# Kernel optimization log

Hardware: AMD Instinct MI355X
Metric: run time of the kernel (lower is better)

Reference implementation:

```python
import jax, jax.numpy as jnp
import numpy as np

N = 50000      # nodes
E = 800000     # edges
G = 64         # graphs in batch
DIN = 128
H = 128
DOUT = 128
EPS = 1e-5     # BatchNorm eps
SLOPE = 0.01   # leaky_relu negative slope


def setup_inputs() -> dict:
    key = jax.random.key(0)
    ks = jax.random.split(key, 12)
    x = jax.random.normal(ks[0], (N, DIN), jnp.float32)
    edge_index = jax.random.randint(ks[1], (2, E), 0, N)
    batch = jnp.sort(jax.random.randint(ks[2], (N,), 0, G))
    edge_weight = jax.random.uniform(ks[3], (E,), jnp.float32)

    def lin(k, i, o):
        return (jax.random.normal(k, (i, o), jnp.float32) / np.float32(np.sqrt(i)))

    W0, b0 = lin(ks[4], DIN, H), jnp.zeros((H,), jnp.float32)
    W1, b1 = lin(ks[5], H, H), jnp.zeros((H,), jnp.float32)
    W2, b2 = lin(ks[6], H, DOUT), jnp.zeros((DOUT,), jnp.float32)
    # BatchNorm (eval mode): affine params + running stats
    g0, be0 = jnp.ones((H,), jnp.float32), jnp.zeros((H,), jnp.float32)
    m0 = 0.1 * jax.random.normal(ks[7], (H,), jnp.float32)
    v0 = jax.random.uniform(ks[8], (H,), jnp.float32, minval=0.5, maxval=1.5)
    g1, be1 = jnp.ones((H,), jnp.float32), jnp.zeros((H,), jnp.float32)
    m1 = 0.1 * jax.random.normal(ks[9], (H,), jnp.float32)
    v1 = jax.random.uniform(ks[10], (H,), jnp.float32, minval=0.5, maxval=1.5)
    return dict(x=x, edge_weight=edge_weight, W0=W0, b0=b0, W1=W1, b1=b1,
                W2=W2, b2=b2, g0=g0, be0=be0, m0=m0, v0=v0,
                g1=g1, be1=be1, m1=m1, v1=v1,
                edge_index=edge_index, batch=batch)


def _gcn_conv(x, src, dst, w, W, b):
    # PyG GCNConv: x' = D^{-1/2}(A + I)D^{-1/2} (x W) + b, self-loop weight 1.
    x = x @ W                                   # [N, out]
    deg = jax.ops.segment_sum(w, dst, num_segments=N)          # [N]
    safe = jnp.where(deg > 0, deg, 1.0)
    dinv = jnp.where(deg > 0, 1.0 / jnp.sqrt(safe), 0.0)        # deg^{-1/2}, inf->0
    norm = dinv[src] * w * dinv[dst]                             # [E+N]
    msgs = x[src] * norm[:, None]                                # [E+N, out]
    return jax.ops.segment_sum(msgs, dst, num_segments=N) + b


def _bn_eval(x, g, b, m, v):
    return (x - m) * jax.lax.rsqrt(v + EPS) * g + b


def _leaky(x):
    return jnp.where(x > 0, x, SLOPE * x)


def reference(x, edge_weight, W0, b0, W1, b1, W2, b2,
              g0, be0, m0, v0, g1, be1, m1, v1, edge_index, batch):
    loops = jnp.arange(N)
    src = jnp.concatenate([edge_index[0], loops])
    dst = jnp.concatenate([edge_index[1], loops])
    w = jnp.concatenate([edge_weight, jnp.ones((N,), edge_weight.dtype)])

    h = _leaky(_bn_eval(_gcn_conv(x, src, dst, w, W0, b0), g0, be0, m0, v0))
    h = _leaky(_bn_eval(_gcn_conv(h, src, dst, w, W1, b1), g1, be1, m1, v1))
    h = _gcn_conv(h, src, dst, w, W2, b2)                        # [N, DOUT]

    # global_mean_pool over batch assignment
    sums = jax.ops.segment_sum(h, batch, num_segments=G)         # [G, DOUT]
    cnt = jax.ops.segment_sum(jnp.ones((N,), h.dtype), batch, num_segments=G)
    return sums / jnp.clip(cnt, 1.0)[:, None]
```

## Files before the change

kernel.cpp:

```cpp
#include <hip/hip_runtime.h>

#define EPS 1e-5f
#define SLOPE 0.01f
#define FIXP 262144.0f
#define RSTRIDE 64

typedef short short8 __attribute__((ext_vector_type(8)));
typedef float f32x4 __attribute__((ext_vector_type(4)));
typedef float f32x2 __attribute__((ext_vector_type(2)));

static __device__ __forceinline__ unsigned short f32_to_bf16(float x){
  unsigned int u = __float_as_uint(x);
  unsigned int r = u + 0x7FFFu + ((u >> 16) & 1u);
  return (unsigned short)(r >> 16);
}
static __device__ __forceinline__ float bf16lo_to_f32(unsigned int v){
  return __uint_as_float(v << 16);
}
static __device__ __forceinline__ float bf16hi_to_f32(unsigned int v){
  return __uint_as_float(v & 0xFFFF0000u);
}


__global__ void k_packzero(const float* __restrict__ W0, const float* __restrict__ W1,
                           const float* __restrict__ W2, short* __restrict__ Bh,
                           short* __restrict__ Bl, unsigned int* __restrict__ cnt,
                           int n){
  if ((int)blockIdx.x >= 192){
    int idx = ((int)blockIdx.x - 192)*256 + threadIdx.x;
    if (idx < n) cnt[idx] = 0u;
    return;
  }
  int idx = blockIdx.x*256 + threadIdx.x;
  int which = idx >> 14;
  int r = idx & 16383;
  const float* W = (which == 0) ? W0 : ((which == 1) ? W1 : W2);
  int j = r & 7;
  int l = (r >> 3) & 63;
  int s = (r >> 9) & 3;
  int t = r >> 11;
  int k = s*32 + ((l >> 4) << 3) + j;
  int nn = t*16 + (l & 15);
  float v = W[k*128 + nn];
  unsigned short hb = f32_to_bf16(v);
  float hf = bf16lo_to_f32(hb);
  unsigned short lb = f32_to_bf16(v - hf);
  Bh[idx] = (short)hb;
  Bl[idx] = (short)lb;
}


__global__ __launch_bounds__(256) void k_fused0(
    const int* __restrict__ dst, const float* __restrict__ ew,
    unsigned int* __restrict__ cnt, int* __restrict__ pwr, int E, int cntB,
    const float* __restrict__ X, const short* __restrict__ Bh,
    const short* __restrict__ Bl, unsigned short* __restrict__ Y, int nrows){
  int bid = (int)blockIdx.x;
  if (bid < cntB){
    int e = bid*256 + (int)threadIdx.x;
    if (e < E){
      unsigned int add = (1u << 24) | (unsigned int)(ew[e] * FIXP);
      unsigned int old = atomicAdd(&cnt[dst[e]], add);
      pwr[e] = (int)(old >> 24);
    }
    return;
  }
  int w    = threadIdx.x >> 6;
  int lane = threadIdx.x & 63;
  int m    = lane & 15;
  int kg   = lane >> 4;
  int row0 = (bid - cntB)*64 + w*16;

  f32x4 acc[8];
  #pragma unroll
  for (int t = 0; t < 8; ++t) acc[t] = (f32x4){0.f, 0.f, 0.f, 0.f};

  int arow = row0 + m;
  if (arow >= nrows) arow = nrows - 1;
  const float* ap0 = X + (size_t)arow*128 + (kg << 3);
  const short8* bh0 = (const short8*)Bh + lane;
  const short8* bl0 = (const short8*)Bl + lane;

  #pragma unroll
  for (int s = 0; s < 4; ++s){
    const float* ap = ap0 + s*32;
    float4 a0 = *(const float4*)ap;
    float4 a1 = *(const float4*)(ap + 4);
    float av[8] = {a0.x, a0.y, a0.z, a0.w, a1.x, a1.y, a1.z, a1.w};
    short8 ah, al;
    #pragma unroll
    for (int j = 0; j < 8; ++j){
      unsigned short hb = f32_to_bf16(av[j]);
      float hf = bf16lo_to_f32(hb);
      ah[j] = (short)hb;
      al[j] = (short)f32_to_bf16(av[j] - hf);
    }
    #pragma unroll
    for (int t = 0; t < 8; ++t){
      short8 bh = bh0[t*256 + s*64];
      short8 bl = bl0[t*256 + s*64];
      acc[t] = __builtin_amdgcn_mfma_f32_16x16x32_bf16(ah, bh, acc[t], 0, 0, 0);
      acc[t] = __builtin_amdgcn_mfma_f32_16x16x32_bf16(al, bh, acc[t], 0, 0, 0);
      acc[t] = __builtin_amdgcn_mfma_f32_16x16x32_bf16(ah, bl, acc[t], 0, 0, 0);
    }
  }
  #pragma unroll
  for (int t = 0; t < 8; ++t){
    #pragma unroll
    for (int r = 0; r < 4; ++r){
      int grow = row0 + (kg << 2) + r;
      if (grow < nrows) Y[(size_t)grow*128 + t*16 + m] = f32_to_bf16(acc[t][r]);
    }
  }
}


__global__ void k_fill(const int* __restrict__ src, const int* __restrict__ dst,
                       const float* __restrict__ w, const int* __restrict__ pwr,
                       const unsigned int* __restrict__ cnt,
                       int2* __restrict__ csr, int E){
  int e = blockIdx.x*blockDim.x + threadIdx.x;
  if (e >= E) return;
  int d = dst[e], s = src[e];
  int slot = pwr[e];
  unsigned int cd = cnt[d], cs = cnt[s];
  float dgd = 1.0f + (float)(cd & 0xFFFFFFu) * (1.0f/FIXP);
  float dgs = 1.0f + (float)(cs & 0xFFFFFFu) * (1.0f/FIXP);
  float nr = rsqrtf(dgd) * rsqrtf(dgs) * w[e];
  if (slot < RSTRIDE)
    csr[((size_t)d << 6) + slot] = make_int2(s, __float_as_int(nr));
}


#define ACC4(v, nn) \
  acc[0] += (f32x2){bf16lo_to_f32((v).x), bf16hi_to_f32((v).x)} * (nn); \
  acc[1] += (f32x2){bf16lo_to_f32((v).y), bf16hi_to_f32((v).y)} * (nn); \
  acc[2] += (f32x2){bf16lo_to_f32((v).z), bf16hi_to_f32((v).z)} * (nn); \
  acc[3] += (f32x2){bf16lo_to_f32((v).w), bf16hi_to_f32((v).w)} * (nn);

template<bool BN>
__global__ __launch_bounds__(256) void k_gather(
    const unsigned short* __restrict__ Y, const unsigned int* __restrict__ cnt,
    const int2* __restrict__ csr,
    const float* __restrict__ bias,
    const float* __restrict__ gam, const float* __restrict__ bet,
    const float* __restrict__ mean, const float* __restrict__ var,
    unsigned int* __restrict__ outv, int n){
  int wid  = (blockIdx.x * blockDim.x + threadIdx.x) >> 6;
  int lane = threadIdx.x & 63;
  if (wid >= n) return;
  int g = lane >> 4;
  int q = lane & 15;

  unsigned int cw = cnt[wid];
  int len = (int)(cw >> 24);
  if (len > RSTRIDE) len = RSTRIDE;
  int lenr = (len + 15) & ~15;

  int cex = 0, cey = 0;
  if (lane < lenr){
    int2 ce = csr[((size_t)wid << 6) + lane];
    cex = ce.x; cey = ce.y;
  }

  f32x2 acc[4];
  #pragma unroll
  for (int j = 0; j < 4; ++j) acc[j] = (f32x2){0.f, 0.f};

  const char* Yb = (const char*)Y;

  for (int base = 0; base < len; base += 16){
    #pragma unroll
    for (int u = 0; u < 4; ++u){
      int j = base + g*4 + u;
      bool valid = j < len;
      int sj = __shfl(cex, j, 64);
      int nj = __shfl(cey, j, 64);
      unsigned su = valid ? (unsigned)sj : 0u;
      float nr = valid ? __int_as_float(nj) : 0.f;
      uint4 v = *(const uint4*)(Yb + ((size_t)su << 8) + (q << 4));
      ACC4(v, nr);
    }
  }

  float s[8] = {acc[0].x, acc[0].y, acc[1].x, acc[1].y,
                acc[2].x, acc[2].y, acc[3].x, acc[3].y};
  #pragma unroll
  for (int j = 0; j < 8; ++j){
    s[j] += __shfl_xor(s[j], 16, 64);
    s[j] += __shfl_xor(s[j], 32, 64);
  }

  if (g == 0){
    uint4 v = *(const uint4*)(Yb + ((size_t)wid << 8) + (q << 4));
    float dg = 1.0f + (float)(cw & 0xFFFFFFu) * (1.0f/FIXP);
    float sf = 1.0f / dg;
    s[0] += bf16lo_to_f32(v.x)*sf; s[1] += bf16hi_to_f32(v.x)*sf;
    s[2] += bf16lo_to_f32(v.y)*sf; s[3] += bf16hi_to_f32(v.y)*sf;
    s[4] += bf16lo_to_f32(v.z)*sf; s[5] += bf16hi_to_f32(v.z)*sf;
    s[6] += bf16lo_to_f32(v.w)*sf; s[7] += bf16hi_to_f32(v.w)*sf;

    int c = q << 3;
    float4 bi0 = *(const float4*)&bias[c];
    float4 bi1 = *(const float4*)&bias[c+4];
    float o[8] = {s[0]+bi0.x, s[1]+bi0.y, s[2]+bi0.z, s[3]+bi0.w,
                  s[4]+bi1.x, s[5]+bi1.y, s[6]+bi1.z, s[7]+bi1.w};
    if (BN){
      float4 ga0 = *(const float4*)&gam[c],  ga1 = *(const float4*)&gam[c+4];
      float4 bt0 = *(const float4*)&bet[c],  bt1 = *(const float4*)&bet[c+4];
      float4 mn0 = *(const float4*)&mean[c], mn1 = *(const float4*)&mean[c+4];
      float4 vr0 = *(const float4*)&var[c],  vr1 = *(const float4*)&var[c+4];
      float gv[8] = {ga0.x,ga0.y,ga0.z,ga0.w, ga1.x,ga1.y,ga1.z,ga1.w};
      float bv[8] = {bt0.x,bt0.y,bt0.z,bt0.w, bt1.x,bt1.y,bt1.z,bt1.w};
      float mv[8] = {mn0.x,mn0.y,mn0.z,mn0.w, mn1.x,mn1.y,mn1.z,mn1.w};
      float vv[8] = {vr0.x,vr0.y,vr0.z,vr0.w, vr1.x,vr1.y,vr1.z,vr1.w};
      #pragma unroll
      for (int j = 0; j < 8; ++j){
        float a = gv[j] * rsqrtf(vv[j] + EPS);
        float tt = (o[j] - mv[j]) * a + bv[j];
        o[j] = tt > 0.f ? tt : SLOPE*tt;
      }
    }
    unsigned int p0 = ((unsigned int)f32_to_bf16(o[1]) << 16) | f32_to_bf16(o[0]);
    unsigned int p1 = ((unsigned int)f32_to_bf16(o[3]) << 16) | f32_to_bf16(o[2]);
    unsigned int p2 = ((unsigned int)f32_to_bf16(o[5]) << 16) | f32_to_bf16(o[4]);
    unsigned int p3 = ((unsigned int)f32_to_bf16(o[7]) << 16) | f32_to_bf16(o[6]);
    *(uint4*)((char*)outv + ((size_t)wid << 8) + (q << 4)) = make_uint4(p0,p1,p2,p3);
  }
}


__global__ __launch_bounds__(256) void k_gemm_bf16(const unsigned short* __restrict__ Xb,
                                                   const short* __restrict__ Bh,
                                                   const short* __restrict__ Bl,
                                                   unsigned short* __restrict__ Y,
                                                   int nrows){
  int w    = threadIdx.x >> 6;
  int lane = threadIdx.x & 63;
  int m    = lane & 15;
  int kg   = lane >> 4;
  int row0 = blockIdx.x*64 + w*16;

  f32x4 acc[8];
  #pragma unroll
  for (int t = 0; t < 8; ++t) acc[t] = (f32x4){0.f, 0.f, 0.f, 0.f};

  int arow = row0 + m;
  if (arow >= nrows) arow = nrows - 1;
  const short8* ap = (const short8*)(Xb + (size_t)arow*128) + kg;
  const short8* bh0 = (const short8*)Bh + lane;
  const short8* bl0 = (const short8*)Bl + lane;

  #pragma unroll
  for (int s = 0; s < 4; ++s){
    short8 a = ap[s*4];
    #pragma unroll
    for (int t = 0; t < 8; ++t){
      acc[t] = __builtin_amdgcn_mfma_f32_16x16x32_bf16(a, bh0[t*256 + s*64], acc[t], 0, 0, 0);
      acc[t] = __builtin_amdgcn_mfma_f32_16x16x32_bf16(a, bl0[t*256 + s*64], acc[t], 0, 0, 0);
    }
  }
  #pragma unroll
  for (int t = 0; t < 8; ++t){
    #pragma unroll
    for (int r = 0; r < 4; ++r){
      int grow = row0 + (kg << 2) + r;
      if (grow < nrows) Y[(size_t)grow*128 + t*16 + m] = f32_to_bf16(acc[t][r]);
    }
  }
}


__global__ void k_pool(const unsigned int* __restrict__ h, const int* __restrict__ batch,
                       float* __restrict__ out, int n){
  __shared__ float2 red[1024];
  __shared__ int ss[2];
  int g = blockIdx.x;
  if (threadIdx.x < 2){
    int target = g + (int)threadIdx.x;
    int lo = 0, hi = n;
    while (lo < hi){ int mid = (lo + hi) >> 1; if (batch[mid] < target) lo = mid + 1; else hi = mid; }
    ss[threadIdx.x] = lo;
  }
  __syncthreads();
  int a = ss[0], b = ss[1];
  int rg = threadIdx.x >> 6;
  int c2 = threadIdx.x & 63;
  float sx = 0.f, sy = 0.f;
  for (int i = a + rg; i < b; i += 16){
    unsigned int v = h[((size_t)i << 6) + c2];
    sx += bf16lo_to_f32(v);
    sy += bf16hi_to_f32(v);
  }
  red[threadIdx.x] = make_float2(sx, sy);
  __syncthreads();
  if (rg == 0){
    float tx = 0.f, ty = 0.f;
    #pragma unroll
    for (int k = 0; k < 16; ++k){
      float2 r = red[c2 + k*64];
      tx += r.x; ty += r.y;
    }
    int cn = b - a;
    float inv = 1.0f / (float)(cn > 0 ? cn : 1);
    out[g*128 + 2*c2]     = tx * inv;
    out[g*128 + 2*c2 + 1] = ty * inv;
  }
}


extern "C" void kernel_launch(void* const* d_in, const int* in_sizes, int n_in,
                              void* d_out, int out_size, void* d_ws, size_t ws_size,
                              hipStream_t stream) {
  const int N = in_sizes[0] / 128;
  const int E = in_sizes[1];
  const int G = out_size / 128;
  const int NB = (N + 255) / 256;
  const int CB = (E + 255) / 256;
  const int GB = (N + 63) / 64;

  const float* x   = (const float*)d_in[0];
  const float* ew  = (const float*)d_in[1];
  const float* W0  = (const float*)d_in[2];
  const float* b0  = (const float*)d_in[3];
  const float* W1  = (const float*)d_in[4];
  const float* b1  = (const float*)d_in[5];
  const float* W2  = (const float*)d_in[6];
  const float* b2  = (const float*)d_in[7];
  const float* g0  = (const float*)d_in[8];
  const float* be0 = (const float*)d_in[9];
  const float* m0  = (const float*)d_in[10];
  const float* v0  = (const float*)d_in[11];
  const float* g1  = (const float*)d_in[12];
  const float* be1 = (const float*)d_in[13];
  const float* m1  = (const float*)d_in[14];
  const float* v1  = (const float*)d_in[15];
  const int*   ei  = (const int*)d_in[16];
  const int*   bat = (const int*)d_in[17];
  float* out = (float*)d_out;

  char* p = (char*)d_ws;
  auto alloc = [&](size_t bytes)->char*{
    char* q = p; p += (bytes + 255) & ~(size_t)255; return q;
  };
  unsigned int* cnt = (unsigned int*)alloc((size_t)N*4);
  int*   pwr    = (int*)  alloc((size_t)E*4);
  int2*  csr    = (int2*) alloc((size_t)N*RSTRIDE*8);
  unsigned short* Y  = (unsigned short*)alloc((size_t)N*128*2);
  unsigned short* Hb = (unsigned short*)alloc((size_t)N*128*2);
  short* Bh = (short*)alloc(3*16384*2);
  short* Bl = (short*)alloc(3*16384*2);

  const int* src = ei;
  const int* dst = ei + E;

  k_packzero<<<192 + NB, 256, 0, stream>>>(W0, W1, W2, Bh, Bl, cnt, N);
  k_fused0<<<CB + GB, 256, 0, stream>>>(dst, ew, cnt, pwr, E, CB, x, Bh, Bl, Y, N);
  k_fill  <<<CB, 256, 0, stream>>>(src, dst, ew, pwr, cnt, csr, E);

  k_gather<true><<<(N+3)/4, 256, 0, stream>>>(Y, cnt, csr,
                                              b0, g0, be0, m0, v0, (unsigned int*)Hb, N);
  k_gemm_bf16<<<GB, 256, 0, stream>>>(Hb, Bh + 16384, Bl + 16384, Y, N);
  k_gather<true><<<(N+3)/4, 256, 0, stream>>>(Y, cnt, csr,
                                              b1, g1, be1, m1, v1, (unsigned int*)Hb, N);
  k_gemm_bf16<<<GB, 256, 0, stream>>>(Hb, Bh + 32768, Bl + 32768, Y, N);
  k_gather<false><<<(N+3)/4, 256, 0, stream>>>(Y, cnt, csr,
                                               b2, nullptr, nullptr, nullptr, nullptr,
                                               (unsigned int*)Hb, N);
  k_pool<<<G, 1024, 0, stream>>>((const unsigned int*)Hb, bat, out, N);
}
```

Measured before the change: 240.7 us.

## Rebalance kernel fusion: separate atomics, fuse CSR fill with GEMM, two nodes per gather wave

The degree/slot atomic pass becomes its own kernel with four edges per thread, and the CSR fill is merged into the first GEMM launch. Both use nontemporal loads and stores. The gather kernel now handles two destination nodes per wavefront and issues both nodes' row loads before accumulating, which raises memory-level parallelism. The costs are higher register pressure in the gather and load imbalance when neighbour counts differ between the paired nodes.

```diff
diff --git a/kernel.cpp b/kernel.cpp
--- a/kernel.cpp
+++ b/kernel.cpp
@@ -50,26 +50,57 @@
 }
 
 
-__global__ __launch_bounds__(256) void k_fused0(
+__global__ __launch_bounds__(256) void k_atomic(
     const int* __restrict__ dst, const float* __restrict__ ew,
-    unsigned int* __restrict__ cnt, int* __restrict__ pwr, int E, int cntB,
+    unsigned int* __restrict__ cnt, int* __restrict__ pwr, int E){
+  int base = blockIdx.x*1024 + (int)threadIdx.x;
+  #pragma unroll
+  for (int u = 0; u < 4; ++u){
+    int e = base + u*256;
+    if (e < E){
+      unsigned int add = (1u << 24) | (unsigned int)(ew[e] * FIXP);
+      unsigned int old = atomicAdd(&cnt[dst[e]], add);
+      __builtin_nontemporal_store((int)(old >> 24), pwr + e);
+    }
+  }
+}
+
+
+__global__ __launch_bounds__(256) void k_fillgemm(
+    const int* __restrict__ src, const int* __restrict__ dst,
+    const float* __restrict__ w, const int* __restrict__ pwr,
+    const unsigned int* __restrict__ cnt, long long* __restrict__ csr,
+    int E, int fillB,
     const float* __restrict__ X, const short* __restrict__ Bh,
     const short* __restrict__ Bl, unsigned short* __restrict__ Y, int nrows){
   int bid = (int)blockIdx.x;
-  if (bid < cntB){
-    int e = bid*256 + (int)threadIdx.x;
-    if (e < E){
-      unsigned int add = (1u << 24) | (unsigned int)(ew[e] * FIXP);
-      unsigned int old = atomicAdd(&cnt[dst[e]], add);
-      pwr[e] = (int)(old >> 24);
+  if (bid < fillB){
+    #pragma unroll
+    for (int u = 0; u < 2; ++u){
+      int e = bid*512 + u*256 + (int)threadIdx.x;
+      if (e < E){
+        int d = __builtin_nontemporal_load(dst + e);
+        int s = __builtin_nontemporal_load(src + e);
+        int slot = __builtin_nontemporal_load(pwr + e);
+        float wv = __builtin_nontemporal_load(w + e);
+        unsigned int cd = cnt[d], cs = cnt[s];
+        float dgd = 1.0f + (float)(cd & 0xFFFFFFu) * (1.0f/FIXP);
+        float dgs = 1.0f + (float)(cs & 0xFFFFFFu) * (1.0f/FIXP);
+        float nr = rsqrtf(dgd) * rsqrtf(dgs) * wv;
+        if (slot < RSTRIDE){
+          long long pk = ((long long)(unsigned)__float_as_int(nr) << 32) |
+                         (unsigned long long)(unsigned)s;
+          __builtin_nontemporal_store(pk, csr + ((size_t)d << 6) + slot);
+        }
+      }
     }
     return;
   }
-  int w    = threadIdx.x >> 6;
+  int wv2  = threadIdx.x >> 6;
   int lane = threadIdx.x & 63;
   int m    = lane & 15;
   int kg   = lane >> 4;
-  int row0 = (bid - cntB)*64 + w*16;
+  int row0 = (bid - fillB)*64 + wv2*16;
 
   f32x4 acc[8];
   #pragma unroll
@@ -115,24 +146,7 @@
 }
 
 
-__global__ void k_fill(const int* __restrict__ src, const int* __restrict__ dst,
-                       const float* __restrict__ w, const int* __restrict__ pwr,
-                       const unsigned int* __restrict__ cnt,
-                       int2* __restrict__ csr, int E){
-  int e = blockIdx.x*blockDim.x + threadIdx.x;
-  if (e >= E) return;
-  int d = dst[e], s = src[e];
-  int slot = pwr[e];
-  unsigned int cd = cnt[d], cs = cnt[s];
-  float dgd = 1.0f + (float)(cd & 0xFFFFFFu) * (1.0f/FIXP);
-  float dgs = 1.0f + (float)(cs & 0xFFFFFFu) * (1.0f/FIXP);
-  float nr = rsqrtf(dgd) * rsqrtf(dgs) * w[e];
-  if (slot < RSTRIDE)
-    csr[((size_t)d << 6) + slot] = make_int2(s, __float_as_int(nr));
-}
-
-
-#define ACC4(v, nn) \
+#define ACC4V(acc, v, nn) \
   acc[0] += (f32x2){bf16lo_to_f32((v).x), bf16hi_to_f32((v).x)} * (nn); \
   acc[1] += (f32x2){bf16lo_to_f32((v).y), bf16hi_to_f32((v).y)} * (nn); \
   acc[2] += (f32x2){bf16lo_to_f32((v).z), bf16hi_to_f32((v).z)} * (nn); \
@@ -146,52 +160,81 @@
     const float* __restrict__ gam, const float* __restrict__ bet,
     const float* __restrict__ mean, const float* __restrict__ var,
     unsigned int* __restrict__ outv, int n){
-  int wid  = (blockIdx.x * blockDim.x + threadIdx.x) >> 6;
+  int wv   = (blockIdx.x*256 + threadIdx.x) >> 6;
   int lane = threadIdx.x & 63;
-  if (wid >= n) return;
+  int nA = wv << 1;
+  if (nA >= n) return;
+  int nB = nA + 1;
+  bool hasB = nB < n;
   int g = lane >> 4;
   int q = lane & 15;
 
-  unsigned int cw = cnt[wid];
-  int len = (int)(cw >> 24);
-  if (len > RSTRIDE) len = RSTRIDE;
-  int lenr = (len + 15) & ~15;
-
-  int cex = 0, cey = 0;
-  if (lane < lenr){
-    int2 ce = csr[((size_t)wid << 6) + lane];
-    cex = ce.x; cey = ce.y;
-  }
-
-  f32x2 acc[4];
-  #pragma unroll
-  for (int j = 0; j < 4; ++j) acc[j] = (f32x2){0.f, 0.f};
+  unsigned int cwA = cnt[nA];
+  unsigned int cwB = hasB ? cnt[nB] : 0u;
+  int lenA = (int)(cwA >> 24); if (lenA > RSTRIDE) lenA = RSTRIDE;
+  int lenB = (int)(cwB >> 24); if (lenB > RSTRIDE) lenB = RSTRIDE;
+
+  int axs = 0, ays = 0, bxs = 0, bys = 0;
+  if (lane < lenA){ int2 e = csr[((size_t)nA << 6) + lane]; axs = e.x; ays = e.y; }
+  if (lane < lenB){ int2 e = csr[((size_t)nB << 6) + lane]; bxs = e.x; bys = e.y; }
+
+  f32x2 aA[4], aB[4];
+  #pragma unroll
+  for (int j = 0; j < 4; ++j){ aA[j] = (f32x2){0.f,0.f}; aB[j] = (f32x2){0.f,0.f}; }
 
   const char* Yb = (const char*)Y;
-
-  for (int base = 0; base < len; base += 16){
+  int lenM = lenA > lenB ? lenA : lenB;
+
+  for (int base = 0; base < lenM; base += 16){
+    uint4 vA[4], vB[4];
+    float nrA[4], nrB[4];
     #pragma unroll
     for (int u = 0; u < 4; ++u){
       int j = base + g*4 + u;
-      bool valid = j < len;
-      int sj = __shfl(cex, j, 64);
-      int nj = __shfl(cey, j, 64);
-      unsigned su = valid ? (unsigned)sj : 0u;
-      float nr = valid ? __int_as_float(nj) : 0.f;
-      uint4 v = *(const uint4*)(Yb + ((size_t)su << 8) + (q << 4));
-      ACC4(v, nr);
-    }
-  }
-
-  float s[8] = {acc[0].x, acc[0].y, acc[1].x, acc[1].y,
-                acc[2].x, acc[2].y, acc[3].x, acc[3].y};
+      {
+        bool val = j < lenA;
+        int sj = __shfl(axs, j, 64);
+        int nj = __shfl(ays, j, 64);
+        unsigned su = val ? (unsigned)sj : 0u;
+        nrA[u] = val ? __int_as_float(nj) : 0.f;
+        vA[u] = *(const uint4*)(Yb + ((size_t)su << 8) + (q << 4));
+      }
+      {
+        bool val = j < lenB;
+        int sj = __shfl(bxs, j, 64);
+        int nj = __shfl(bys, j, 64);
+        unsigned su = val ? (unsigned)sj : 0u;
+        nrB[u] = val ? __int_as_float(nj) : 0.f;
+        vB[u] = *(const uint4*)(Yb + ((size_t)su << 8) + (q << 4));
+      }
+    }
+    #pragma unroll
+    for (int u = 0; u < 4; ++u){
+      ACC4V(aA, vA[u], nrA[u]);
+      ACC4V(aB, vB[u], nrB[u]);
+    }
+  }
+
+  float sA[8] = {aA[0].x, aA[0].y, aA[1].x, aA[1].y,
+                 aA[2].x, aA[2].y, aA[3].x, aA[3].y};
+  float sB[8] = {aB[0].x, aB[0].y, aB[1].x, aB[1].y,
+                 aB[2].x, aB[2].y, aB[3].x, aB[3].y};
   #pragma unroll
   for (int j = 0; j < 8; ++j){
-    s[j] += __shfl_xor(s[j], 16, 64);
-    s[j] += __shfl_xor(s[j], 32, 64);
-  }
-
-  if (g == 0){
+    sA[j] += __shfl_xor(sA[j], 16, 64);
+    sA[j] += __shfl_xor(sA[j], 32, 64);
+    sB[j] += __shfl_xor(sB[j], 16, 64);
+    sB[j] += __shfl_xor(sB[j], 32, 64);
+  }
+
+  if (g == 0 || (g == 1 && hasB)){
+    bool isB = (g == 1);
+    int wid = isB ? nB : nA;
+    unsigned int cw = isB ? cwB : cwA;
+    float s[8];
+    #pragma unroll
+    for (int j = 0; j < 8; ++j) s[j] = isB ? sB[j] : sA[j];
+
     uint4 v = *(const uint4*)(Yb + ((size_t)wid << 8) + (q << 4));
     float dg = 1.0f + (float)(cw & 0xFFFFFFu) * (1.0f/FIXP);
     float sf = 1.0f / dg;
@@ -316,7 +359,8 @@
   const int E = in_sizes[1];
   const int G = out_size / 128;
   const int NB = (N + 255) / 256;
-  const int CB = (E + 255) / 256;
+  const int AB = (E + 1023) / 1024;
+  const int FB = (E + 511) / 512;
   const int GB = (N + 63) / 64;
 
   const float* x   = (const float*)d_in[0];
@@ -355,16 +399,17 @@
   const int* dst = ei + E;
 
   k_packzero<<<192 + NB, 256, 0, stream>>>(W0, W1, W2, Bh, Bl, cnt, N);
-  k_fused0<<<CB + GB, 256, 0, stream>>>(dst, ew, cnt, pwr, E, CB, x, Bh, Bl, Y, N);
-  k_fill  <<<CB, 256, 0, stream>>>(src, dst, ew, pwr, cnt, csr, E);
-
-  k_gather<true><<<(N+3)/4, 256, 0, stream>>>(Y, cnt, csr,
+  k_atomic  <<<AB, 256, 0, stream>>>(dst, ew, cnt, pwr, E);
+  k_fillgemm<<<FB + GB, 256, 0, stream>>>(src, dst, ew, pwr, cnt, (long long*)csr,
+                                          E, FB, x, Bh, Bl, Y, N);
+
+  k_gather<true><<<(N+7)/8, 256, 0, stream>>>(Y, cnt, csr,
                                               b0, g0, be0, m0, v0, (unsigned int*)Hb, N);
   k_gemm_bf16<<<GB, 256, 0, stream>>>(Hb, Bh + 16384, Bl + 16384, Y, N);
-  k_gather<true><<<(N+3)/4, 256, 0, stream>>>(Y, cnt, csr,
+  k_gather<true><<<(N+7)/8, 256, 0, stream>>>(Y, cnt, csr,
                                               b1, g1, be1, m1, v1, (unsigned int*)Hb, N);
   k_gemm_bf16<<<GB, 256, 0, stream>>>(Hb, Bh + 32768, Bl + 32768, Y, N);
-  k_gather<false><<<(N+3)/4, 256, 0, stream>>>(Y, cnt, csr,
+  k_gather<false><<<(N+7)/8, 256, 0, stream>>>(Y, cnt, csr,
                                                b2, nullptr, nullptr, nullptr, nullptr,
                                                (unsigned int*)Hb, N);
   k_pool<<<G, 1024, 0, stream>>>((const unsigned int*)Hb, bat, out, N);
```

After: 253.7 us. +5.4%, slower.

## Fuse GCN gather+BN+leaky with next-layer GEMM via LDS staging

Applied to the files above, without the earlier changes.

Merges each hidden layer's neighbour gather, bias/BatchNorm/leaky-ReLU epilogue and the following weight GEMM into a single 512-thread kernel. Each block gathers 64 rows into shared memory as bf16, then runs MFMA against the next layer's split-bf16 weights. This removes two kernel launches and the global write and re-read of the intermediate activation. The cost is lower gather parallelism, since each wave now handles 8 rows serially in a block that also synchronises, which may reduce latency hiding for the irregular gathers.

```diff
diff --git a/kernel.cpp b/kernel.cpp
--- a/kernel.cpp
+++ b/kernel.cpp
@@ -131,20 +131,142 @@
     csr[((size_t)d << 6) + slot] = make_int2(s, __float_as_int(nr));
 }
 
-
 #define ACC4(v, nn) \
   acc[0] += (f32x2){bf16lo_to_f32((v).x), bf16hi_to_f32((v).x)} * (nn); \
   acc[1] += (f32x2){bf16lo_to_f32((v).y), bf16hi_to_f32((v).y)} * (nn); \
   acc[2] += (f32x2){bf16lo_to_f32((v).z), bf16hi_to_f32((v).z)} * (nn); \
   acc[3] += (f32x2){bf16lo_to_f32((v).w), bf16hi_to_f32((v).w)} * (nn);
 
-template<bool BN>
-__global__ __launch_bounds__(256) void k_gather(
+
+__global__ __launch_bounds__(512) void k_gatherW(
     const unsigned short* __restrict__ Y, const unsigned int* __restrict__ cnt,
     const int2* __restrict__ csr,
     const float* __restrict__ bias,
     const float* __restrict__ gam, const float* __restrict__ bet,
     const float* __restrict__ mean, const float* __restrict__ var,
+    const short* __restrict__ Bh, const short* __restrict__ Bl,
+    unsigned short* __restrict__ Yout, int n){
+  __shared__ char lds[64*264];
+  int w    = threadIdx.x >> 6;
+  int lane = threadIdx.x & 63;
+  int g = lane >> 4;
+  int q = lane & 15;
+  int blk = blockIdx.x;
+  const char* Yb = (const char*)Y;
+
+  for (int i = 0; i < 8; ++i){
+    int lr = w*8 + i;
+    int wid = blk*64 + lr;
+    if (wid < n){
+      unsigned int cw = cnt[wid];
+      int len = (int)(cw >> 24);
+      if (len > RSTRIDE) len = RSTRIDE;
+      int lenr = (len + 15) & ~15;
+      int cex = 0, cey = 0;
+      if (lane < lenr){
+        int2 ce = csr[((size_t)wid << 6) + lane];
+        cex = ce.x; cey = ce.y;
+      }
+      f32x2 acc[4];
+      #pragma unroll
+      for (int j = 0; j < 4; ++j) acc[j] = (f32x2){0.f, 0.f};
+      for (int base = 0; base < len; base += 16){
+        #pragma unroll
+        for (int u = 0; u < 4; ++u){
+          int j = base + g*4 + u;
+          bool valid = j < len;
+          int sj = __shfl(cex, j, 64);
+          int nj = __shfl(cey, j, 64);
+          unsigned su = valid ? (unsigned)sj : 0u;
+          float nr = valid ? __int_as_float(nj) : 0.f;
+          uint4 v = *(const uint4*)(Yb + ((size_t)su << 8) + (q << 4));
+          ACC4(v, nr);
+        }
+      }
+      float s[8] = {acc[0].x, acc[0].y, acc[1].x, acc[1].y,
+                    acc[2].x, acc[2].y, acc[3].x, acc[3].y};
+      #pragma unroll
+      for (int j = 0; j < 8; ++j){
+        s[j] += __shfl_xor(s[j], 16, 64);
+        s[j] += __shfl_xor(s[j], 32, 64);
+      }
+      if (g == 0){
+        uint4 v = *(const uint4*)(Yb + ((size_t)wid << 8) + (q << 4));
+        float dg = 1.0f + (float)(cw & 0xFFFFFFu) * (1.0f/FIXP);
+        float sf = 1.0f / dg;
+        s[0] += bf16lo_to_f32(v.x)*sf; s[1] += bf16hi_to_f32(v.x)*sf;
+        s[2] += bf16lo_to_f32(v.y)*sf; s[3] += bf16hi_to_f32(v.y)*sf;
+        s[4] += bf16lo_to_f32(v.z)*sf; s[5] += bf16hi_to_f32(v.z)*sf;
+        s[6] += bf16lo_to_f32(v.w)*sf; s[7] += bf16hi_to_f32(v.w)*sf;
+        int c = q << 3;
+        float4 bi0 = *(const float4*)&bias[c];
+        float4 bi1 = *(const float4*)&bias[c+4];
+        float o[8] = {s[0]+bi0.x, s[1]+bi0.y, s[2]+bi0.z, s[3]+bi0.w,
+                      s[4]+bi1.x, s[5]+bi1.y, s[6]+bi1.z, s[7]+bi1.w};
+        float4 ga0 = *(const float4*)&gam[c],  ga1 = *(const float4*)&gam[c+4];
+        float4 bt0 = *(const float4*)&bet[c],  bt1 = *(const float4*)&bet[c+4];
+        float4 mn0 = *(const float4*)&mean[c], mn1 = *(const float4*)&mean[c+4];
+        float4 vr0 = *(const float4*)&var[c],  vr1 = *(const float4*)&var[c+4];
+        float gv[8] = {ga0.x,ga0.y,ga0.z,ga0.w, ga1.x,ga1.y,ga1.z,ga1.w};
+        float bv[8] = {bt0.x,bt0.y,bt0.z,bt0.w, bt1.x,bt1.y,bt1.z,bt1.w};
+        float mv[8] = {mn0.x,mn0.y,mn0.z,mn0.w, mn1.x,mn1.y,mn1.z,mn1.w};
+        float vv[8] = {vr0.x,vr0.y,vr0.z,vr0.w, vr1.x,vr1.y,vr1.z,vr1.w};
+        #pragma unroll
+        for (int j = 0; j < 8; ++j){
+          float a = gv[j] * rsqrtf(vv[j] + EPS);
+          float tt = (o[j] - mv[j]) * a + bv[j];
+          o[j] = tt > 0.f ? tt : SLOPE*tt;
+        }
+        unsigned int p0 = ((unsigned int)f32_to_bf16(o[1]) << 16) | f32_to_bf16(o[0]);
+        unsigned int p1 = ((unsigned int)f32_to_bf16(o[3]) << 16) | f32_to_bf16(o[2]);
+        unsigned int p2 = ((unsigned int)f32_to_bf16(o[5]) << 16) | f32_to_bf16(o[4]);
+        unsigned int p3 = ((unsigned int)f32_to_bf16(o[7]) << 16) | f32_to_bf16(o[6]);
+        *(uint4*)(lds + lr*264 + (q << 4)) = make_uint4(p0,p1,p2,p3);
+      }
+    } else if (g == 0){
+      *(uint4*)(lds + lr*264 + (q << 4)) = make_uint4(0,0,0,0);
+    }
+  }
+  __syncthreads();
+
+  int tr = w & 3;
+  int tc = w >> 1 & ~0;
+  int ch = w >> 2;
+  int m  = lane & 15;
+  int kg = lane >> 4;
+
+  f32x4 acc4[4];
+  #pragma unroll
+  for (int t = 0; t < 4; ++t) acc4[t] = (f32x4){0.f, 0.f, 0.f, 0.f};
+
+  const char* arow = lds + (tr*16 + m)*264 + (kg << 4);
+  const short8* bh0 = (const short8*)Bh;
+  const short8* bl0 = (const short8*)Bl;
+
+  #pragma unroll
+  for (int s = 0; s < 4; ++s){
+    short8 a = *(const short8*)(arow + s*64);
+    #pragma unroll
+    for (int t = 0; t < 4; ++t){
+      int tt = ch*4 + t;
+      acc4[t] = __builtin_amdgcn_mfma_f32_16x16x32_bf16(a, bh0[tt*256 + s*64 + lane], acc4[t], 0, 0, 0);
+      acc4[t] = __builtin_amdgcn_mfma_f32_16x16x32_bf16(a, bl0[tt*256 + s*64 + lane], acc4[t], 0, 0, 0);
+    }
+  }
+  #pragma unroll
+  for (int t = 0; t < 4; ++t){
+    #pragma unroll
+    for (int r = 0; r < 4; ++r){
+      int grow = blk*64 + tr*16 + (kg << 2) + r;
+      if (grow < n) Yout[(size_t)grow*128 + (ch*4 + t)*16 + m] = f32_to_bf16(acc4[t][r]);
+    }
+  }
+}
+
+
+__global__ __launch_bounds__(256) void k_gather_last(
+    const unsigned short* __restrict__ Y, const unsigned int* __restrict__ cnt,
+    const int2* __restrict__ csr, const float* __restrict__ bias,
     unsigned int* __restrict__ outv, int n){
   int wid  = (blockIdx.x * blockDim.x + threadIdx.x) >> 6;
   int lane = threadIdx.x & 63;
@@ -199,74 +321,16 @@
     s[2] += bf16lo_to_f32(v.y)*sf; s[3] += bf16hi_to_f32(v.y)*sf;
     s[4] += bf16lo_to_f32(v.z)*sf; s[5] += bf16hi_to_f32(v.z)*sf;
     s[6] += bf16lo_to_f32(v.w)*sf; s[7] += bf16hi_to_f32(v.w)*sf;
-
     int c = q << 3;
     float4 bi0 = *(const float4*)&bias[c];
     float4 bi1 = *(const float4*)&bias[c+4];
     float o[8] = {s[0]+bi0.x, s[1]+bi0.y, s[2]+bi0.z, s[3]+bi0.w,
                   s[4]+bi1.x, s[5]+bi1.y, s[6]+bi1.z, s[7]+bi1.w};
-    if (BN){
-      float4 ga0 = *(const float4*)&gam[c],  ga1 = *(const float4*)&gam[c+4];
-      float4 bt0 = *(const float4*)&bet[c],  bt1 = *(const float4*)&bet[c+4];
-      float4 mn0 = *(const float4*)&mean[c], mn1 = *(const float4*)&mean[c+4];
-      float4 vr0 = *(const float4*)&var[c],  vr1 = *(const float4*)&var[c+4];
-      float gv[8] = {ga0.x,ga0.y,ga0.z,ga0.w, ga1.x,ga1.y,ga1.z,ga1.w};
-      float bv[8] = {bt0.x,bt0.y,bt0.z,bt0.w, bt1.x,bt1.y,bt1.z,bt1.w};
-      float mv[8] = {mn0.x,mn0.y,mn0.z,mn0.w, mn1.x,mn1.y,mn1.z,mn1.w};
-      float vv[8] = {vr0.x,vr0.y,vr0.z,vr0.w, vr1.x,vr1.y,vr1.z,vr1.w};
-      #pragma unroll
-      for (int j = 0; j < 8; ++j){
-        float a = gv[j] * rsqrtf(vv[j] + EPS);
-        float tt = (o[j] - mv[j]) * a + bv[j];
-        o[j] = tt > 0.f ? tt : SLOPE*tt;
-      }
-    }
     unsigned int p0 = ((unsigned int)f32_to_bf16(o[1]) << 16) | f32_to_bf16(o[0]);
     unsigned int p1 = ((unsigned int)f32_to_bf16(o[3]) << 16) | f32_to_bf16(o[2]);
     unsigned int p2 = ((unsigned int)f32_to_bf16(o[5]) << 16) | f32_to_bf16(o[4]);
     unsigned int p3 = ((unsigned int)f32_to_bf16(o[7]) << 16) | f32_to_bf16(o[6]);
     *(uint4*)((char*)outv + ((size_t)wid << 8) + (q << 4)) = make_uint4(p0,p1,p2,p3);
-  }
-}
-
-
-__global__ __launch_bounds__(256) void k_gemm_bf16(const unsigned short* __restrict__ Xb,
-                                                   const short* __restrict__ Bh,
-                                                   const short* __restrict__ Bl,
-                                                   unsigned short* __restrict__ Y,
-                                                   int nrows){
-  int w    = threadIdx.x >> 6;
-  int lane = threadIdx.x & 63;
-  int m    = lane & 15;
-  int kg   = lane >> 4;
-  int row0 = blockIdx.x*64 + w*16;
-
-  f32x4 acc[8];
-  #pragma unroll
-  for (int t = 0; t < 8; ++t) acc[t] = (f32x4){0.f, 0.f, 0.f, 0.f};
-
-  int arow = row0 + m;
-  if (arow >= nrows) arow = nrows - 1;
-  const short8* ap = (const short8*)(Xb + (size_t)arow*128) + kg;
-  const short8* bh0 = (const short8*)Bh + lane;
-  const short8* bl0 = (const short8*)Bl + lane;
-
-  #pragma unroll
-  for (int s = 0; s < 4; ++s){
-    short8 a = ap[s*4];
-    #pragma unroll
-    for (int t = 0; t < 8; ++t){
-      acc[t] = __builtin_amdgcn_mfma_f32_16x16x32_bf16(a, bh0[t*256 + s*64], acc[t], 0, 0, 0);
-      acc[t] = __builtin_amdgcn_mfma_f32_16x16x32_bf16(a, bl0[t*256 + s*64], acc[t], 0, 0, 0);
-    }
-  }
-  #pragma unroll
-  for (int t = 0; t < 8; ++t){
-    #pragma unroll
-    for (int r = 0; r < 4; ++r){
-      int grow = row0 + (kg << 2) + r;
-      if (grow < nrows) Y[(size_t)grow*128 + t*16 + m] = f32_to_bf16(acc[t][r]);
-    }
   }
 }
 
@@ -358,14 +422,10 @@
   k_fused0<<<CB + GB, 256, 0, stream>>>(dst, ew, cnt, pwr, E, CB, x, Bh, Bl, Y, N);
   k_fill  <<<CB, 256, 0, stream>>>(src, dst, ew, pwr, cnt, csr, E);
 
-  k_gather<true><<<(N+3)/4, 256, 0, stream>>>(Y, cnt, csr,
-                                              b0, g0, be0, m0, v0, (unsigned int*)Hb, N);
-  k_gemm_bf16<<<GB, 256, 0, stream>>>(Hb, Bh + 16384, Bl + 16384, Y, N);
-  k_gather<true><<<(N+3)/4, 256, 0, stream>>>(Y, cnt, csr,
-                                              b1, g1, be1, m1, v1, (unsigned int*)Hb, N);
-  k_gemm_bf16<<<GB, 256, 0, stream>>>(Hb, Bh + 32768, Bl + 32768, Y, N);
-  k_gather<false><<<(N+3)/4, 256, 0, stream>>>(Y, cnt, csr,
-                                               b2, nullptr, nullptr, nullptr, nullptr,
-                                               (unsigned int*)Hb, N);
+  k_gatherW<<<GB, 512, 0, stream>>>(Y, cnt, csr, b0, g0, be0, m0, v0,
+                                    Bh + 16384, Bl + 16384, Hb, N);
+  k_gatherW<<<GB, 512, 0, stream>>>(Hb, cnt, csr, b1, g1, be1, m1, v1,
+                                    Bh + 32768, Bl + 32768, Y, N);
+  k_gather_last<<<(N+3)/4, 256, 0, stream>>>(Y, cnt, csr, b2, (unsigned int*)Hb, N);
   k_pool<<<G, 1024, 0, stream>>>((const unsigned int*)Hb, bat, out, N);
 }
```

Result: no change. 240.8 us (+0.0%).
